# Kernel optimization log

Hardware: AMD Instinct MI355X
Metric: run time of the kernel (lower is better)

## Reference

```python
import jax, jax.numpy as jnp
import numpy as np
import math

B, S, U, H = 8, 1024, 1024, 16
DK = U // H  # 64


def setup_inputs() -> dict:
    key = jax.random.key(0)
    ks = jax.random.split(key, 12)
    query = jax.random.normal(ks[0], (B, S, U), jnp.float32)
    key_t = jax.random.normal(ks[1], (B, S, U), jnp.float32)  # unused by module (bug preserved)
    value = jax.random.normal(ks[2], (B, S, U), jnp.float32)  # unused by module (bug preserved)
    # causal multiplicative 0/1 mask [B,S,S]
    mask = jnp.broadcast_to(jnp.tril(jnp.ones((S, S), jnp.float32)), (B, S, S))
    bh = math.sqrt(1.0 / DK)   # init bound for per-head projections (out_features=d_k)
    bo = math.sqrt(1.0 / U)    # init bound for output projection (out_features=n_units)
    u = lambda k, shape, b: jax.random.uniform(k, shape, jnp.float32, -b, b)
    # per-head weights stacked: [H, U, DK] (already input->output layout)
    Wq = u(ks[3], (H, U, DK), bh); bq = u(ks[4], (H, DK), bh)
    Wk = u(ks[5], (H, U, DK), bh); bk = u(ks[6], (H, DK), bh)
    Wv = u(ks[7], (H, U, DK), bh); bv = u(ks[8], (H, DK), bh)
    Wo = u(ks[9], (U, U), bo);     bo_ = u(ks[10], (U,), bo)
    return dict(query=query, key=key_t, value=value, mask=mask,
                Wq=Wq, bq=bq, Wk=Wk, bk=bk, Wv=Wv, bv=bv, Wo=Wo, bo=bo_)


def reference(query, key, value, mask, Wq, bq, Wk, bk, Wv, bv, Wo, bo):
    # NOTE: faithful to source — q, k, v are ALL projected from `query`.
    q = jnp.einsum('bsu,hud->bhsd', query, Wq) + bq[:, None, :]
    k = jnp.einsum('bsu,hud->bhsd', query, Wk) + bk[:, None, :]
    v = jnp.einsum('bsu,hud->bhsd', query, Wv) + bv[:, None, :]
    scores = jnp.einsum('bhqd,bhkd->bhqk', q, k) / math.sqrt(DK)
    s = mask[:, None, :, :]  # broadcast over heads
    x = scores * s - 1e9 * (1.0 - s)  # multiplicative mask baked into softmax input
    attn = jax.nn.softmax(x, axis=-1)
    out = jnp.einsum('bhqk,bhkd->bhqd', attn, v)
    # concat heads along feature dim (head 0 first, matching torch.cat order)
    out = out.transpose(0, 2, 1, 3).reshape(B, S, U)
    return out @ Wo + bo
```

## Files before the change

kernel.cpp:

```cpp
#include <hip/hip_runtime.h>
#include <hip/hip_bf16.h>

#define B_ 8
#define S_ 1024
#define U_ 1024
#define H_ 16
#define DK_ 64

typedef __attribute__((ext_vector_type(8))) short short8;
typedef __attribute__((ext_vector_type(4))) float f32x4;
typedef __attribute__((ext_vector_type(16))) float f32x16;

__device__ inline ushort f2b(float x) {
  union { float f; unsigned u; } v; v.f = x;
  unsigned r = (v.u + 0x7FFFu + ((v.u >> 16) & 1u)) >> 16;
  return (ushort)r;
}
__device__ inline unsigned cvtpk(float lo, float hi) {
  unsigned r;
  asm("v_cvt_pk_bf16_f32 %0, %1, %2" : "=v"(r) : "v"(lo), "v"(hi));
  return r;
}

__device__ inline void gld16(const ushort* g, ushort* l) {
  __builtin_amdgcn_global_load_lds((__attribute__((address_space(1))) void*)(g),
                                   (__attribute__((address_space(3))) void*)(l),
                                   16, 0, 0);
}

__global__ __launch_bounds__(256) void pack_all_kern(
    const float* __restrict__ X, ushort* __restrict__ Xb,
    const float* __restrict__ Wq, const float* __restrict__ Wk, const float* __restrict__ Wv,
    const float* __restrict__ bq, const float* __restrict__ bk, const float* __restrict__ bv,
    const float* __restrict__ Wo,
    ushort* __restrict__ Wqkv, float* __restrict__ Bqkv, ushort* __restrict__ Wob)
{
  __shared__ ushort tile[64*65];
  const int t = threadIdx.x;
  if (blockIdx.x < 4096) {
    int idx = blockIdx.x * 256 + t;
    const float4* src = (const float4*)X + (size_t)idx * 2;
    float4 a = src[0], b = src[1];
    ushort r[8];
    r[0]=f2b(a.x); r[1]=f2b(a.y); r[2]=f2b(a.z); r[3]=f2b(a.w);
    r[4]=f2b(b.x); r[5]=f2b(b.y); r[6]=f2b(b.z); r[7]=f2b(b.w);
    *(uint4*)(Xb + (size_t)idx*8) = *(uint4*)r;
    return;
  }
  const int bid = blockIdx.x - 4096;
  if (bid < 768) {
    int p = bid >> 8, rem = bid & 255;
    int h = rem >> 4, kc = rem & 15, k0 = kc*64;
    const float* Wsrc = (p==0) ? Wq : ((p==1) ? Wk : Wv);
    #pragma unroll
    for (int i = 0; i < 16; ++i) {
      int e = t + i*256;
      int r = e >> 6, d = e & 63;
      tile[d*65 + r] = f2b(Wsrc[h*65536 + (k0+r)*64 + d]);
    }
    __syncthreads();
    #pragma unroll
    for (int i = 0; i < 16; ++i) {
      int e = t + i*256;
      int d = e >> 6, r = e & 63;
      Wqkv[(size_t)(p*1024 + h*64 + d)*1024 + k0 + r] = tile[d*65 + r];
    }
    if (kc == 0 && t < 64) {
      const float* bsrc = (p==0) ? bq : ((p==1) ? bk : bv);
      Bqkv[p*1024 + h*64 + t] = bsrc[h*64 + t];
    }
  } else {
    int b2 = bid - 768;
    int nc = b2 >> 4, kc = b2 & 15;
    int n0 = nc*64, k0 = kc*64;
    #pragma unroll
    for (int i = 0; i < 16; ++i) {
      int e = t + i*256;
      int r = e >> 6, d = e & 63;
      tile[d*65 + r] = f2b(Wo[(size_t)(k0+r)*1024 + n0 + d]);
    }
    __syncthreads();
    #pragma unroll
    for (int i = 0; i < 16; ++i) {
      int e = t + i*256;
      int d = e >> 6, r = e & 63;
      Wob[(size_t)(n0+d)*1024 + k0 + r] = tile[d*65 + r];
    }
  }
}

__global__ __launch_bounds__(256, 2) void gemmw_kern(
    const ushort* __restrict__ A,
    const ushort* __restrict__ Bw,
    const float* __restrict__ bias,
    ushort* __restrict__ Qb, ushort* __restrict__ Kb, ushort* __restrict__ Vtb)
{
  __shared__ __align__(16) ushort As[3][8192];
  __shared__ __align__(16) ushort Bs[3][4096];

  const int t = threadIdx.x;
  const int l = t & 63, w = t >> 6;
  const int wr = w >> 1, wc = w & 1;
  const int li = l & 15, c4 = l >> 4;

  const int swz = (blockIdx.x & 7) * 96 + (blockIdx.x >> 3);
  const int ms = swz / 96, rem = swz % 96;
  const int m0 = (ms*4 + (rem & 3)) * 256;
  const int n0 = (rem >> 2) * 128;

  f32x4 acc[8][4];
  #pragma unroll
  for (int i=0;i<8;i++)
    #pragma unroll
    for (int j=0;j<4;j++) acc[i][j] = (f32x4)0.0f;

  auto SA = [&](int buf, int kk) {
    #pragma unroll
    for (int p2=0;p2<4;++p2) {
      int n = p2*256 + t;
      int row = n >> 2, jj = (n & 3) ^ ((row >> 1) & 3);
      gld16(&A[(size_t)(m0 + row)*1024 + kk + jj*8], &As[buf][n*8]);
    }
  };
  auto SB = [&](int buf, int kk) {
    #pragma unroll
    for (int p2=0;p2<2;++p2) {
      int n = p2*256 + t;
      int row = n >> 2, jj = (n & 3) ^ ((row >> 1) & 3);
      gld16(&Bw[(size_t)(n0 + row)*1024 + kk + jj*8], &Bs[buf][n*8]);
    }
  };

  SA(0, 0);  SB(0, 0);
  SA(1, 32); SB(1, 32);

  for (int kt = 0; kt < 32; ++kt) {
    const int cur = kt % 3;
    asm volatile("s_waitcnt vmcnt(6)" ::: "memory");
    __builtin_amdgcn_s_barrier();
    __builtin_amdgcn_sched_barrier(0);

    short8 af[8], bf[4];
    #pragma unroll
    for (int i=0;i<8;i++) {
      int rA = wr*128 + i*16 + li;
      af[i] = *(const short8*)&As[cur][rA*32 + ((c4 ^ ((rA>>1)&3))*8)];
    }
    #pragma unroll
    for (int j=0;j<4;j++) {
      int rB = wc*64 + j*16 + li;
      bf[j] = *(const short8*)&Bs[cur][rB*32 + ((c4 ^ ((rB>>1)&3))*8)];
    }
    __builtin_amdgcn_s_barrier();
    __builtin_amdgcn_sched_barrier(0);
    const int nb = (kt + 2) % 3;
    const int kk2 = ((kt + 2) & 31) * 32;
    SA(nb, kk2); SB(nb, kk2);

    __builtin_amdgcn_s_setprio(1);
    #pragma unroll
    for (int i=0;i<8;i++)
      #pragma unroll
      for (int j=0;j<4;j++)
        acc[i][j] = __builtin_amdgcn_mfma_f32_16x16x32_bf16(af[i], bf[j], acc[i][j], 0,0,0);
    __builtin_amdgcn_s_setprio(0);
  }

  #pragma unroll
  for (int i=0;i<8;i++) {
    int rbase = m0 + wr*128 + i*16 + c4*4;
    #pragma unroll
    for (int j=0;j<4;j++) {
      int col = n0 + wc*64 + j*16 + li;
      float bv = bias[col];
      int p = col >> 10, h = (col >> 6) & 15, d = col & 63;
      int b = rbase >> 10, s = rbase & 1023;
      if (p == 2) {
        unsigned pk4[2];
        pk4[0] = cvtpk(acc[i][j][0] + bv, acc[i][j][1] + bv);
        pk4[1] = cvtpk(acc[i][j][2] + bv, acc[i][j][3] + bv);
        *(uint2*)&Vtb[((size_t)((b*16+h)*64 + d))*1024 + s] = *(uint2*)pk4;
      } else {
        ushort* dst = (p==0) ? Qb : Kb;
        float sc = (p==0) ? 0.18033688011112042f : 1.0f;
        #pragma unroll
        for (int r=0;r<4;r++)
          dst[(((size_t)(b*16 + h))*1024 + s + r)*64 + d] = f2b((acc[i][j][r] + bv) * sc);
      }
    }
  }
}

template<int MODE>
__global__ __launch_bounds__(256, 3) void gemm128_kern(
    const ushort* __restrict__ A,
    const ushort* __restrict__ Bw,
    const float* __restrict__ bias,
    ushort* __restrict__ Qb, ushort* __restrict__ Kb, ushort* __restrict__ Vtb,
    float* __restrict__ outF)
{
  __shared__ __align__(16) ushort As[3][4096];
  __shared__ __align__(16) ushort Bs[3][4096];

  const int t = threadIdx.x;
  const int l = t & 63, w = t >> 6;
  const int wr = w >> 1, wc = w & 1;
  const int li = l & 15, c4 = l >> 4;

  int m0, n0;
  {
    int swz = (blockIdx.x & 7) * 64 + (blockIdx.x >> 3);
    int ms = swz / 64, rem = swz % 64;
    m0 = (ms*8 + (rem & 7)) * 128;  n0 = (rem >> 3) * 128;
  }

  f32x4 acc[4][4];
  #pragma unroll
  for (int i=0;i<4;i++)
    #pragma unroll
    for (int j=0;j<4;j++) acc[i][j] = (f32x4)0.0f;

  auto SA = [&](int buf, int kk) {
    #pragma unroll
    for (int p2=0;p2<2;++p2) {
      int n = p2*256 + t;
      int row = n >> 2, jj = (n & 3) ^ ((row >> 1) & 3);
      gld16(&A[(size_t)(m0 + row)*1024 + kk + jj*8], &As[buf][n*8]);
    }
  };
  auto SB = [&](int buf, int kk) {
    #pragma unroll
    for (int p2=0;p2<2;++p2) {
      int n = p2*256 + t;
      int row = n >> 2, jj = (n & 3) ^ ((row >> 1) & 3);
      gld16(&Bw[(size_t)(n0 + row)*1024 + kk + jj*8], &Bs[buf][n*8]);
    }
  };

  SA(0, 0);  SB(0, 0);
  SA(1, 32); SB(1, 32);

  for (int kt = 0; kt < 32; ++kt) {
    const int cur = kt % 3;
    asm volatile("s_waitcnt vmcnt(4)" ::: "memory");
    __builtin_amdgcn_s_barrier();
    __builtin_amdgcn_sched_barrier(0);

    short8 af[4], bf[4];
    #pragma unroll
    for (int i=0;i<4;i++) {
      int rA = wr*64 + i*16 + li;
      int rB = wc*64 + i*16 + li;
      af[i] = *(const short8*)&As[cur][rA*32 + ((c4 ^ ((rA>>1)&3))*8)];
      bf[i] = *(const short8*)&Bs[cur][rB*32 + ((c4 ^ ((rB>>1)&3))*8)];
    }
    __builtin_amdgcn_s_barrier();
    __builtin_amdgcn_sched_barrier(0);
    const int nb = (kt + 2) % 3;
    const int kk2 = ((kt + 2) & 31) * 32;
    SA(nb, kk2); SB(nb, kk2);

    __builtin_amdgcn_s_setprio(1);
    #pragma unroll
    for (int i=0;i<4;i++)
      #pragma unroll
      for (int j=0;j<4;j++)
        acc[i][j] = __builtin_amdgcn_mfma_f32_16x16x32_bf16(af[i], bf[j], acc[i][j], 0,0,0);
    __builtin_amdgcn_s_setprio(0);
  }

  #pragma unroll
  for (int i=0;i<4;i++) {
    int rbase = m0 + wr*64 + i*16 + c4*4;
    #pragma unroll
    for (int j=0;j<4;j++) {
      int col = n0 + wc*64 + j*16 + li;
      float bv = bias[col];
      #pragma unroll
      for (int r=0;r<4;r++)
        outF[(size_t)(rbase+r)*1024 + col] = acc[i][j][r] + bv;
    }
  }
}

__global__ __launch_bounds__(256, 2) void attn_kern(
    const ushort* __restrict__ Qb, const ushort* __restrict__ Kb,
    const ushort* __restrict__ Vt, ushort* __restrict__ Ob)
{
  __shared__ __align__(16) ushort Ks[2][32*68];
  __shared__ __align__(16) ushort Vs[2][64*44];
  __shared__ __align__(16) ushort Pb[4][32*40];
  __shared__ __align__(16) ushort OT[4][32*72];
  const int t = threadIdx.x, l = t & 63, w = t >> 6;
  const int bid = blockIdx.x;
  const int x = bid & 7, i0 = bid >> 3;
  const int bh = x*16 + (i0 >> 2);
  const int g  = i0 & 3;
  const int p  = g*4 + w;
  const int qta = p, qtb = 31 - p;
  const int NT = 32 - g*4;

  const int col = l & 31, hi = l >> 5;
  const ushort* Qp = Qb + (size_t)bh*65536;
  const ushort* Kp = Kb + (size_t)bh*65536;
  const ushort* Vp = Vt + (size_t)bh*65536;

  const int ks_row = t >> 3, ks_c = t & 7;
  const int vs_row = t >> 2, vs_c = t & 3;

  short8 qfa[4], qfb[4];
  #pragma unroll
  for (int m=0;m<4;m++) {
    qfa[m] = *(const short8*)&Qp[(size_t)(qta*32+col)*64 + m*16 + hi*8];
    qfb[m] = *(const short8*)&Qp[(size_t)(qtb*32+col)*64 + m*16 + hi*8];
  }

  f32x16 aA0 = (f32x16)0.0f, aA1 = (f32x16)0.0f;
  f32x16 aB0 = (f32x16)0.0f, aB1 = (f32x16)0.0f;
  float mA = -1e30f, lA = 0.0f, mB = -1e30f, lB = 0.0f;
  ushort* Pw = &Pb[w][0];

  auto PROC = [&](f32x16& s, bool diag, float& mR, float& lS,
                  f32x16& o0, f32x16& o1, const short8* vf0, const short8* vf1) {
    if (diag) {
      #pragma unroll
      for (int r=0;r<16;r++) {
        int kvl = (r&3) + ((r>>2)<<3) + 4*hi;
        s[r] = (kvl > col) ? -1e9f : s[r];
      }
    }
    float t0 = fmaxf(fmaxf(s[0], s[1]), s[2]);
    float t1 = fmaxf(fmaxf(s[3], s[4]), s[5]);
    float t2 = fmaxf(fmaxf(s[6], s[7]), s[8]);
    float t3 = fmaxf(fmaxf(s[9], s[10]), s[11]);
    float t4 = fmaxf(fmaxf(s[12], s[13]), s[14]);
    float mx = fmaxf(fmaxf(fmaxf(t0, t1), t2), fmaxf(fmaxf(t3, t4), s[15]));
    mx = fmaxf(mx, __shfl_xor(mx, 32));
    if (__any(mx - mR > 8.0f)) {
      float mN = fmaxf(mR, mx);
      float corr = __builtin_amdgcn_exp2f(mR - mN);
      mR = mN; lS *= corr;
      #pragma unroll
      for (int r=0;r<16;r++) { o0[r] *= corr; o1[r] *= corr; }
    }
    float pr[16];
    #pragma unroll
    for (int r=0;r<16;r++) pr[r] = __builtin_amdgcn_exp2f(s[r] - mR);
    float s8[8];
    #pragma unroll
    for (int r2=0;r2<8;r2++) s8[r2] = pr[2*r2] + pr[2*r2+1];
    #pragma unroll
    for (int r2=0;r2<4;r2++) s8[r2] += s8[r2+4];
    float rs = (s8[0]+s8[1]) + (s8[2]+s8[3]);
    rs += __shfl_xor(rs, 32);
    lS += rs;
    #pragma unroll
    for (int r2=0;r2<8;r2++) {
      int r = 2*r2;
      int kv = (r&3) + ((r>>2)<<3) + 4*hi;
      *(unsigned*)&Pw[col*40 + kv] = cvtpk(pr[r], pr[r+1]);
    }
    short8 pb0 = *(const short8*)&Pw[col*40 + hi*8];
    short8 pb1 = *(const short8*)&Pw[col*40 + 16 + hi*8];
    o0 = __builtin_amdgcn_mfma_f32_32x32x16_bf16(vf0[0], pb0, o0, 0,0,0);
    o0 = __builtin_amdgcn_mfma_f32_32x32x16_bf16(vf0[1], pb1, o0, 0,0,0);
    o1 = __builtin_amdgcn_mfma_f32_32x32x16_bf16(vf1[0], pb0, o1, 0,0,0);
    o1 = __builtin_amdgcn_mfma_f32_32x32x16_bf16(vf1[1], pb1, o1, 0,0,0);
  };

  {
    uint4 k0v = *(const uint4*)&Kp[(size_t)ks_row*64 + ks_c*8];
    uint4 v0v = *(const uint4*)&Vp[(size_t)vs_row*1024 + vs_c*8];
    *(uint4*)&Ks[0][ks_row*68 + ks_c*8] = k0v;
    *(uint4*)&Vs[0][vs_row*44 + vs_c*8] = v0v;
  }
  __syncthreads();

  for (int kt = 0; kt < NT; ++kt) {
    const int cur = kt & 1;
    const bool pre = (kt + 1 < NT);
    uint4 kn2, vn2;
    if (pre) {
      kn2 = *(const uint4*)&Kp[(size_t)((kt+1)*32+ks_row)*64 + ks_c*8];
      vn2 = *(const uint4*)&Vp[(size_t)vs_row*1024 + (kt+1)*32 + vs_c*8];
    }

    short8 kf[4], vf0[2], vf1[2];
    #pragma unroll
    for (int m=0;m<4;m++)
      kf[m] = *(const short8*)&Ks[cur][col*68 + m*16 + hi*8];
    #pragma unroll
    for (int m=0;m<2;m++) {
      vf0[m] = *(const short8*)&Vs[cur][col*44 + m*16 + hi*8];
      vf1[m] = *(const short8*)&Vs[cur][(col+32)*44 + m*16 + hi*8];
    }

    const bool doB = (kt <= qtb), doA = (kt <= qta);
    if (doB) {
      f32x16 sB = (f32x16)0.0f;
      #pragma unroll
      for (int m=0;m<4;m++)
        sB = __builtin_amdgcn_mfma_f32_32x32x16_bf16(kf[m], qfb[m], sB, 0, 0, 0);
      if (doA) {
        f32x16 sA = (f32x16)0.0f;
        #pragma unroll
        for (int m=0;m<4;m++)
          sA = __builtin_amdgcn_mfma_f32_32x32x16_bf16(kf[m], qfa[m], sA, 0, 0, 0);
        PROC(sB, kt == qtb, mB, lB, aB0, aB1, vf0, vf1);
        PROC(sA, kt == qta, mA, lA, aA0, aA1, vf0, vf1);
      } else {
        PROC(sB, kt == qtb, mB, lB, aB0, aB1, vf0, vf1);
      }
    }

    if (pre) {
      *(uint4*)&Ks[cur^1][ks_row*68 + ks_c*8] = kn2;
      *(uint4*)&Vs[cur^1][vs_row*44 + vs_c*8] = vn2;
    }
    __syncthreads();
  }

  const int b = bh >> 4, h = bh & 15;
  auto EPI = [&](int qt, float lS, const f32x16& o0, const f32x16& o1) {
    float inv = 1.0f / lS;
    ushort* o = &OT[w][0];
    #pragma unroll
    for (int r2=0;r2<8;r2++) {
      int r = 2*r2;
      int dv = (r&3) + ((r>>2)<<3) + 4*hi;
      *(unsigned*)&o[col*72 + dv]      = cvtpk(o0[r]*inv, o0[r+1]*inv);
      *(unsigned*)&o[col*72 + 32 + dv] = cvtpk(o1[r]*inv, o1[r+1]*inv);
    }
    #pragma unroll
    for (int it=0; it<4; ++it) {
      int q = it*8 + (l>>3), c8 = (l&7)*8;
      uint4 v = *(const uint4*)&o[q*72 + c8];
      int qg = qt*32 + q;
      *(uint4*)&Ob[(size_t)(b*1024+qg)*1024 + h*64 + c8] = v;
    }
  };
  EPI(qta, lA, aA0, aA1);
  EPI(qtb, lB, aB0, aB1);
}

extern "C" void kernel_launch(void* const* d_in, const int* in_sizes, int n_in,
                              void* d_out, int out_size, void* d_ws, size_t ws_size,
                              hipStream_t stream) {
  const float* query = (const float*)d_in[0];
  const float* Wq = (const float*)d_in[4];
  const float* bq = (const float*)d_in[5];
  const float* Wk = (const float*)d_in[6];
  const float* bk = (const float*)d_in[7];
  const float* Wv = (const float*)d_in[8];
  const float* bv = (const float*)d_in[9];
  const float* Wo = (const float*)d_in[10];
  const float* bo = (const float*)d_in[11];

  char* wsb = (char*)d_ws;
  ushort* Xb   = (ushort*)(wsb);
  ushort* Wqkv = (ushort*)(wsb + 16777216);
  float*  Bqkv = (float*) (wsb + 23068672);
  ushort* Wob  = (ushort*)(wsb + 23080960);
  ushort* Qb   = (ushort*)(wsb + 25178112);
  ushort* Kb   = (ushort*)(wsb + 41955328);
  ushort* Vtb  = (ushort*)(wsb + 58732544);
  ushort* Ob   = (ushort*)(wsb + 75509760);

  hipLaunchKernelGGL(pack_all_kern, dim3(5120), dim3(256), 0, stream,
                     query, Xb, Wq, Wk, Wv, bq, bk, bv, Wo, Wqkv, Bqkv, Wob);
  hipLaunchKernelGGL(gemmw_kern, dim3(768), dim3(256), 0, stream,
                     Xb, Wqkv, Bqkv, Qb, Kb, Vtb);
  hipLaunchKernelGGL(attn_kern, dim3(512), dim3(256), 0, stream, Qb, Kb, Vtb, Ob);
  hipLaunchKernelGGL(gemm128_kern<1>, dim3(512), dim3(256), 0, stream,
                     Ob, Wob, bo, (ushort*)nullptr, (ushort*)nullptr, (ushort*)nullptr,
                     (float*)d_out);
}
```

Measured before the change: 143.1 us.

## Rewrite QKV GEMM as 8-wave 256x256 tile with quadrant-phased ping-pong pipeline

```diff
diff --git a/kernel.cpp b/kernel.cpp
--- a/kernel.cpp
+++ b/kernel.cpp
@@ -89,24 +89,24 @@
   }
 }
 
-__global__ __launch_bounds__(256, 2) void gemmw_kern(
+__global__ __launch_bounds__(512, 2) void gemmw8_kern(
     const ushort* __restrict__ A,
     const ushort* __restrict__ Bw,
     const float* __restrict__ bias,
     ushort* __restrict__ Qb, ushort* __restrict__ Kb, ushort* __restrict__ Vtb)
 {
-  __shared__ __align__(16) ushort As[3][8192];
-  __shared__ __align__(16) ushort Bs[3][4096];
+  __shared__ __align__(16) ushort As[2][2][8192];
+  __shared__ __align__(16) ushort Bs[2][2][8192];
 
   const int t = threadIdx.x;
   const int l = t & 63, w = t >> 6;
-  const int wr = w >> 1, wc = w & 1;
+  const int wr = w >> 2, wc = w & 3;
   const int li = l & 15, c4 = l >> 4;
 
-  const int swz = (blockIdx.x & 7) * 96 + (blockIdx.x >> 3);
-  const int ms = swz / 96, rem = swz % 96;
+  const int swz = (blockIdx.x & 7) * 48 + (blockIdx.x >> 3);
+  const int ms = swz / 48, rem = swz % 48;
   const int m0 = (ms*4 + (rem & 3)) * 256;
-  const int n0 = (rem >> 2) * 128;
+  const int n0 = (rem >> 2) * 256;
 
   f32x4 acc[8][4];
   #pragma unroll
@@ -114,57 +114,77 @@
     #pragma unroll
     for (int j=0;j<4;j++) acc[i][j] = (f32x4)0.0f;
 
-  auto SA = [&](int buf, int kk) {
-    #pragma unroll
-    for (int p2=0;p2<4;++p2) {
-      int n = p2*256 + t;
-      int row = n >> 2, jj = (n & 3) ^ ((row >> 1) & 3);
-      gld16(&A[(size_t)(m0 + row)*1024 + kk + jj*8], &As[buf][n*8]);
-    }
-  };
-  auto SB = [&](int buf, int kk) {
-    #pragma unroll
-    for (int p2=0;p2<2;++p2) {
-      int n = p2*256 + t;
-      int row = n >> 2, jj = (n & 3) ^ ((row >> 1) & 3);
-      gld16(&Bw[(size_t)(n0 + row)*1024 + kk + jj*8], &Bs[buf][n*8]);
-    }
-  };
-
-  SA(0, 0);  SB(0, 0);
-  SA(1, 32); SB(1, 32);
-
-  for (int kt = 0; kt < 32; ++kt) {
-    const int cur = kt % 3;
-    asm volatile("s_waitcnt vmcnt(6)" ::: "memory");
-    __builtin_amdgcn_s_barrier();
-    __builtin_amdgcn_sched_barrier(0);
-
-    short8 af[8], bf[4];
-    #pragma unroll
-    for (int i=0;i<8;i++) {
-      int rA = wr*128 + i*16 + li;
-      af[i] = *(const short8*)&As[cur][rA*32 + ((c4 ^ ((rA>>1)&3))*8)];
-    }
-    #pragma unroll
-    for (int j=0;j<4;j++) {
-      int rB = wc*64 + j*16 + li;
-      bf[j] = *(const short8*)&Bs[cur][rB*32 + ((c4 ^ ((rB>>1)&3))*8)];
-    }
-    __builtin_amdgcn_s_barrier();
-    __builtin_amdgcn_sched_barrier(0);
-    const int nb = (kt + 2) % 3;
-    const int kk2 = ((kt + 2) & 31) * 32;
-    SA(nb, kk2); SB(nb, kk2);
-
-    __builtin_amdgcn_s_setprio(1);
-    #pragma unroll
-    for (int i=0;i<8;i++)
-      #pragma unroll
-      for (int j=0;j<4;j++)
-        acc[i][j] = __builtin_amdgcn_mfma_f32_16x16x32_bf16(af[i], bf[j], acc[i][j], 0,0,0);
-    __builtin_amdgcn_s_setprio(0);
-  }
+  auto SGA = [&](int buf, int qm, int kk) {
+    #pragma unroll
+    for (int u=0;u<2;++u) {
+      int n = u*512 + t;
+      int r = n >> 3, jj = (n & 7) ^ (r & 7);
+      gld16(&A[(size_t)(m0 + (r>>6)*128 + qm*64 + (r&63))*1024 + kk + jj*8],
+            &As[buf][qm][n*8]);
+    }
+  };
+  auto SGB = [&](int buf, int qn, int kk) {
+    #pragma unroll
+    for (int u=0;u<2;++u) {
+      int n = u*512 + t;
+      int r = n >> 3, jj = (n & 7) ^ (r & 7);
+      gld16(&Bw[(size_t)(n0 + (r>>5)*64 + qn*32 + (r&31))*1024 + kk + jj*8],
+            &Bs[buf][qn][n*8]);
+    }
+  };
+
+  SGB(0,0,0); SGA(0,0,0); SGA(0,1,0); SGB(0,1,0); SGB(1,0,64); SGA(1,0,64);
+
+#define PH(BUF, QM, QN, STAGE_STMT)                                           \
+  asm volatile("s_waitcnt vmcnt(8)" ::: "memory");                            \
+  __builtin_amdgcn_s_barrier();                                               \
+  __builtin_amdgcn_sched_barrier(0);                                          \
+  {                                                                           \
+    short8 af[4][2], bf[2][2];                                                \
+    _Pragma("unroll")                                                         \
+    for (int i=0;i<4;i++) {                                                   \
+      int ar = wr*64 + i*16 + li;                                             \
+      _Pragma("unroll")                                                       \
+      for (int ks=0;ks<2;ks++)                                                \
+        af[i][ks] = *(const short8*)&As[BUF][QM][ar*64 + (((ks*4+c4)^(li&7))*8)]; \
+    }                                                                         \
+    _Pragma("unroll")                                                         \
+    for (int jj=0;jj<2;jj++) {                                                \
+      int br = wc*32 + jj*16 + li;                                            \
+      _Pragma("unroll")                                                       \
+      for (int ks=0;ks<2;ks++)                                                \
+        bf[jj][ks] = *(const short8*)&Bs[BUF][QN][br*64 + (((ks*4+c4)^(li&7))*8)]; \
+    }                                                                         \
+    STAGE_STMT;                                                               \
+    asm volatile("s_waitcnt lgkmcnt(0)" ::: "memory");                        \
+    __builtin_amdgcn_sched_barrier(0);                                        \
+    __builtin_amdgcn_s_setprio(1);                                            \
+    _Pragma("unroll")                                                         \
+    for (int i=0;i<4;i++)                                                     \
+      _Pragma("unroll")                                                       \
+      for (int jj=0;jj<2;jj++)                                                \
+        _Pragma("unroll")                                                     \
+        for (int ks=0;ks<2;ks++)                                              \
+          acc[(QM)*4+i][(QN)*2+jj] = __builtin_amdgcn_mfma_f32_16x16x32_bf16( \
+              af[i][ks], bf[jj][ks], acc[(QM)*4+i][(QN)*2+jj], 0,0,0);        \
+    __builtin_amdgcn_s_setprio(0);                                            \
+  }
+
+  #pragma unroll 1
+  for (int it = 0; it < 8; ++it) {
+    const int k1 = (2*it+1)*64;
+    const int k2 = (2*it+2 < 16) ? (2*it+2)*64 : 0;
+    const int k3 = (2*it+3 < 16) ? (2*it+3)*64 : 0;
+    PH(0,0,0, SGA(1,1,k1))
+    PH(0,1,0, SGB(1,1,k1))
+    PH(0,0,1, SGB(0,0,k2))
+    PH(0,1,1, SGA(0,0,k2))
+    PH(1,0,0, SGA(0,1,k2))
+    PH(1,1,0, SGB(0,1,k2))
+    PH(1,0,1, SGB(1,0,k3))
+    PH(1,1,1, SGA(1,0,k3))
+  }
+#undef PH
 
   #pragma unroll
   for (int i=0;i<8;i++) {
@@ -468,7 +488,7 @@
 
   hipLaunchKernelGGL(pack_all_kern, dim3(5120), dim3(256), 0, stream,
                      query, Xb, Wq, Wk, Wv, bq, bk, bv, Wo, Wqkv, Bqkv, Wob);
-  hipLaunchKernelGGL(gemmw_kern, dim3(768), dim3(256), 0, stream,
+  hipLaunchKernelGGL(gemmw8_kern, dim3(384), dim3(512), 0, stream,
                      Xb, Wqkv, Bqkv, Qb, Kb, Vtb);
   hipLaunchKernelGGL(attn_kern, dim3(512), dim3(256), 0, stream, Qb, Kb, Vtb, Ob);
   hipLaunchKernelGGL(gemm128_kern<1>, dim3(512), dim3(256), 0, stream,
```

After: 154.2 us. 7.7% more time.
